# Kernel tuning notes

Measured on AMD Instinct MI355X. Metric: run time of the kernel, lower is better.

Reference implementation:

```python
import jax, jax.numpy as jnp
import numpy as np

B, CIN, CINT, H, W = 2, 2048, 512, 96, 96
CQK = CINT // 8  # 64, mmcv CrissCrossAttention query/key channels
NG = 32          # GroupNorm groups
EPS = 1e-5


def conv1x1(x, w, b):
    # x: [B,C,H,W], w: [O,C,1,1], b: [O]
    y = jnp.einsum('bchw,oc->bohw', x, w[:, :, 0, 0])
    return y + b[None, :, None, None]


def conv3x3(x, w):
    return jax.lax.conv_general_dilated(
        x, w, window_strides=(1, 1), padding=((1, 1), (1, 1)),
        dimension_numbers=('NCHW', 'OIHW', 'NCHW'))


def group_norm(x, gamma, beta):
    b, c, h, w = x.shape
    xg = x.reshape(b, NG, c // NG, h, w)
    mu = xg.mean(axis=(2, 3, 4), keepdims=True)
    var = xg.var(axis=(2, 3, 4), keepdims=True)
    xg = (xg - mu) * jax.lax.rsqrt(var + EPS)
    return xg.reshape(b, c, h, w) * gamma[None, :, None, None] + beta[None, :, None, None]


def criss_cross_attention(x, qw, qb, kw, kb, vw, vb, gamma):
    # mmcv CrissCrossAttention: attention restricted to each pixel's row + column.
    b, c, h, w = x.shape
    q = conv1x1(x, qw, qb)  # [B,Cqk,H,W]
    k = conv1x1(x, kw, kb)  # [B,Cqk,H,W]
    v = conv1x1(x, vw, vb)  # [B,C,H,W]
    # column (H-direction) energy: e_H[b,h,w,i] = sum_c q[b,c,h,w] k[b,c,i,w]
    e_h = jnp.einsum('bchw,bciw->bhwi', q, k)
    diag = jnp.eye(h, dtype=bool)[:, None, :]  # mask i==h (self counted once, in W branch)
    e_h = jnp.where(diag, -jnp.inf, e_h)
    # row (W-direction) energy: e_W[b,h,w,j] = sum_c q[b,c,h,w] k[b,c,h,j]
    e_w = jnp.einsum('bchw,bchj->bhwj', q, k)
    attn = jax.nn.softmax(jnp.concatenate([e_h, e_w], axis=-1), axis=-1)  # [B,H,W,H+W]
    a_h, a_w = attn[..., :h], attn[..., h:]
    out = jnp.einsum('bciw,bhwi->bchw', v, a_h) + jnp.einsum('bchj,bhwj->bchw', v, a_w)
    return gamma * out + x


def setup_inputs() -> dict:
    key = jax.random.key(0)
    ks = jax.random.split(key, 12)
    s = 0.02
    return {
        'x': jax.random.normal(ks[0], (B, CIN, H, W), jnp.float32),
        'conv1_w': jax.random.normal(ks[1], (CINT, CIN, 1, 1), jnp.float32) * s,
        'conv1_b': jnp.zeros((CINT,), jnp.float32),
        'q_w': jax.random.normal(ks[2], (CQK, CINT, 1, 1), jnp.float32) * s,
        'q_b': jnp.zeros((CQK,), jnp.float32),
        'k_w': jax.random.normal(ks[3], (CQK, CINT, 1, 1), jnp.float32) * s,
        'k_b': jnp.zeros((CQK,), jnp.float32),
        'v_w': jax.random.normal(ks[4], (CINT, CINT, 1, 1), jnp.float32) * s,
        'v_b': jnp.zeros((CINT,), jnp.float32),
        'gamma': jnp.asarray(0.5, jnp.float32),
        'convout_w': jax.random.normal(ks[5], (CINT, CINT, 3, 3), jnp.float32) * s,
        'gn_gamma': jnp.ones((CINT,), jnp.float32),
        'gn_beta': jnp.zeros((CINT,), jnp.float32),
    }


def reference(x, conv1_w, conv1_b, q_w, q_b, k_w, k_b, v_w, v_b, gamma,
              convout_w, gn_gamma, gn_beta):
    out = conv1x1(x, conv1_w, conv1_b)
    for _ in range(2):  # recurrence = 2
        out = criss_cross_attention(out, q_w, q_b, k_w, k_b, v_w, v_b, gamma)
    out = conv3x3(out, convout_w)  # ConvModule with GN => conv has no bias
    out = group_norm(out, gn_gamma, gn_beta)
    return out
```

## Files before the change

### kernel.cpp

```cpp
#include <hip/hip_runtime.h>
#include <hip/hip_bf16.h>


typedef __bf16 bf8_t __attribute__((ext_vector_type(8)));
typedef float f32x4 __attribute__((ext_vector_type(4)));

union I4B8 { int4 i; bf8_t b; };

typedef const __attribute__((address_space(1))) void as1_cvoid;
typedef __attribute__((address_space(3))) void as3_void;
__device__ __forceinline__ void gload16(const void* g, void* l) {
  __builtin_amdgcn_global_load_lds((as1_cvoid*)g, (as3_void*)l, 16, 0, 0);
}
__device__ __forceinline__ int rot8(int c, int key) { return (c + key) & 7; }

__global__ __launch_bounds__(256) void cast_rot_k(const float* s, __bf16* d, int K8, int total8) {
  int idx = blockIdx.x * 256 + threadIdx.x;
  if (idx >= total8) return;
  int c8 = idx % K8, n = idx / K8;
  int pos = rot8(c8 & 7, n & 7);
  const float* sp = s + ((long long)n * K8 + c8) * 8;
  float4 a = *(const float4*)sp, b = *(const float4*)(sp + 4);
  I4B8 u;
  u.b[0] = (__bf16)a.x; u.b[1] = (__bf16)a.y; u.b[2] = (__bf16)a.z; u.b[3] = (__bf16)a.w;
  u.b[4] = (__bf16)b.x; u.b[5] = (__bf16)b.y; u.b[6] = (__bf16)b.z; u.b[7] = (__bf16)b.w;
  *(int4*)(d + ((long long)n * K8 + (c8 & ~7) + pos) * 8) = u.i;
}

__global__ __launch_bounds__(256) void wqkv_rot_k(const float* qw, const float* kw, const float* vw, __bf16* d) {
  int idx = blockIdx.x * 256 + threadIdx.x;
  if (idx >= 640 * 64) return;
  int c8 = idx & 63, n = idx >> 6;
  const float* src = (n < 64) ? qw + (long long)n * 512
                   : (n < 128) ? kw + (long long)(n - 64) * 512
                               : vw + (long long)(n - 128) * 512;
  int pos = rot8(c8 & 7, n & 7);
  const float* sp = src + c8 * 8;
  float4 a = *(const float4*)sp, b = *(const float4*)(sp + 4);
  I4B8 u;
  u.b[0] = (__bf16)a.x; u.b[1] = (__bf16)a.y; u.b[2] = (__bf16)a.z; u.b[3] = (__bf16)a.w;
  u.b[4] = (__bf16)b.x; u.b[5] = (__bf16)b.y; u.b[6] = (__bf16)b.z; u.b[7] = (__bf16)b.w;
  *(int4*)(d + ((long long)n * 64 + (c8 & ~7) + pos) * 8) = u.i;
}

__global__ __launch_bounds__(256) void fuse_bias_k(const float* qb, const float* kb, const float* vb, float* d) {
  int i = blockIdx.x * 256 + threadIdx.x;
  if (i >= 640) return;
  d[i] = (i < 64) ? qb[i] : (i < 128) ? kb[i - 64] : vb[i - 128];
}

__global__ __launch_bounds__(256) void reorder_w_k(const float* w, __bf16* wr) {
  __shared__ float ls[4608];
  int o = blockIdx.x;
  int t = threadIdx.x;
  const float* base = w + (long long)o * 4608;
#pragma unroll
  for (int i = 0; i < 18; i++) ls[t + i * 256] = base[t + i * 256];
  __syncthreads();
#pragma unroll
  for (int i = 0; i < 3; i++) {
    int q = t + i * 256;
    if (q >= 576) break;
    int k0 = q * 8;
    int dydx = k0 / 512, c0 = k0 & 511;
    I4B8 u;
#pragma unroll
    for (int j = 0; j < 8; j++) u.b[j] = (__bf16)ls[(c0 + j) * 9 + dydx];
    int pos = rot8((k0 >> 3) & 7, o & 7);
    *(int4*)(wr + (long long)o * 4608 + (k0 & ~63) + pos * 8) = u.i;
  }
}

__global__ __launch_bounds__(256) void transpose_x_k(const float* x, __bf16* xt) {
  __shared__ __bf16 l[64 * 66];
  int c0 = blockIdx.x * 64, s0 = blockIdx.y * 64, b = blockIdx.z;
  int t = threadIdx.x;
#pragma unroll
  for (int i = 0; i < 2; i++) {
    int slot = t + i * 256;
    int cl = slot >> 3, sch = slot & 7;
    const float* src = x + ((long long)(b * 2048 + c0 + cl)) * 9216 + s0 + sch * 8;
    float4 a = *(const float4*)src, bb = *(const float4*)(src + 4);
    __bf16* dst = &l[cl * 66 + sch * 8];
    dst[0] = (__bf16)a.x; dst[1] = (__bf16)a.y; dst[2] = (__bf16)a.z; dst[3] = (__bf16)a.w;
    dst[4] = (__bf16)bb.x; dst[5] = (__bf16)bb.y; dst[6] = (__bf16)bb.z; dst[7] = (__bf16)bb.w;
  }
  __syncthreads();
#pragma unroll
  for (int i = 0; i < 2; i++) {
    int slot = t + i * 256;
    int sl = slot >> 3, cch = slot & 7;
    I4B8 u;
#pragma unroll
    for (int j = 0; j < 8; j++) u.b[j] = l[(cch * 8 + j) * 66 + sl];
    *(int4*)(xt + ((long long)(b * 9216 + s0 + sl)) * 2048 + c0 + rot8(cch, sl & 7) * 8) = u.i;
  }
}

__global__ __launch_bounds__(256) void border0_k(__bf16* padb) {
  int idx = blockIdx.x * 256 + threadIdx.x;
  if (idx >= 776 * 64) return;
  int ch = idx & 63, bi = idx >> 6;
  int b = bi / 388, r = bi % 388;
  int hh, ww;
  if (r < 98) { hh = 0; ww = r; }
  else if (r < 196) { hh = 97; ww = r - 98; }
  else if (r < 292) { hh = r - 196 + 1; ww = 0; }
  else { hh = r - 292 + 1; ww = 97; }
  *(int4*)(padb + ((long long)(b * 9604 + hh * 98 + ww)) * 512 + ch * 8) = make_int4(0, 0, 0, 0);
}

struct GemmAP {
  const __bf16 *A, *B;
  __bf16* C;
  const float* bias;
  long long sAr, sBr, sCr;
  int K, ntn;
};

template <int CROT>
__global__ __launch_bounds__(256) void gemm_async_k(GemmAP p) {
  __shared__ __attribute__((aligned(16))) __bf16 lA[128 * 64];
  __shared__ __attribute__((aligned(16))) __bf16 lB[128 * 64];
  const int t = threadIdx.x;
  const int id = blockIdx.x;
  const int per8 = gridDim.x >> 3;
  const int lin = (id & 7) * per8 + (id >> 3);
  const int m0 = (lin / p.ntn) * 128, n0 = (lin % p.ntn) * 128;
  const int lane = t & 63, wave = t >> 6;
  const int wm = (wave >> 1) * 64, wn = (wave & 1) * 64;
  const int l15 = lane & 15, l4 = lane >> 4;
  const int srow = (lane >> 3), schunk = (lane & 7) * 8;
  f32x4 acc[4][4];
#pragma unroll
  for (int i = 0; i < 4; i++)
#pragma unroll
    for (int j = 0; j < 4; j++) acc[i][j] = f32x4{0.f, 0.f, 0.f, 0.f};

  for (int kb = 0; kb < p.K; kb += 64) {
    const int rb = wave * 32;
#pragma unroll
    for (int i = 0; i < 4; i++) {
      int row = rb + i * 8;
      gload16(p.A + (long long)(m0 + row + srow) * p.sAr + kb + schunk, &lA[row * 64]);
      gload16(p.B + (long long)(n0 + row + srow) * p.sBr + kb + schunk, &lB[row * 64]);
    }
    __syncthreads();
#pragma unroll
    for (int kk = 0; kk < 2; kk++) {
      bf8_t af[4], bfr[4];
      int cch = kk * 4 + l4;
#pragma unroll
      for (int mt = 0; mt < 4; mt++) {
        int r = wm + mt * 16 + l15;
        af[mt] = *(bf8_t*)&lA[r * 64 + (rot8(cch, r & 7) << 3)];
      }
#pragma unroll
      for (int nt = 0; nt < 4; nt++) {
        int r = wn + nt * 16 + l15;
        bfr[nt] = *(bf8_t*)&lB[r * 64 + (rot8(cch, r & 7) << 3)];
      }
#pragma unroll
      for (int mt = 0; mt < 4; mt++)
#pragma unroll
        for (int nt = 0; nt < 4; nt++)
          acc[mt][nt] = __builtin_amdgcn_mfma_f32_16x16x32_bf16(af[mt], bfr[nt], acc[mt][nt], 0, 0, 0);
    }
    __syncthreads();
  }
#pragma unroll
  for (int nt = 0; nt < 4; nt++) {
    int col = n0 + wn + nt * 16 + l15;
    float bv = p.bias[col];
#pragma unroll
    for (int mt = 0; mt < 4; mt++) {
      int row0 = m0 + wm + mt * 16 + (l4 << 2);
#pragma unroll
      for (int r = 0; r < 4; r++) {
        int row = row0 + r;
        int pc = CROT ? (col & ~63) + (rot8((col >> 3) & 7, row & 7) << 3) + (col & 7) : col;
        p.C[(long long)row * p.sCr + pc] = (__bf16)(acc[mt][nt][r] + bv);
      }
    }
  }
}

struct AggP {
  const __bf16 *A, *B;
  __bf16* C;
  const __bf16 *tmp, *res;
  const float* gma;
  long long bB1, bB2, sBr;
  long long cB1, cB2, sCr;
};

template <int MODE>
__global__ __launch_bounds__(256) void agg_k(AggP p) {
  __shared__ __attribute__((aligned(16))) __bf16 lA[128 * 64];
  __shared__ __attribute__((aligned(16))) __bf16 lB[128 * 64];
  const int t = threadIdx.x;
  const int z = blockIdx.z;
  const int z1 = z / 96, z2 = z % 96;
  const __bf16* A = p.A + (long long)z * (96 * 128);
  const __bf16* B = p.B + (long long)z1 * p.bB1 + (long long)z2 * p.bB2;
  const int n0 = blockIdx.x * 128;
  const int lane = t & 63, wave = t >> 6;
  const int wm = (wave >> 1) * 64, wn = (wave & 1) * 64;
  const int l15 = lane & 15, l4 = lane >> 4;
  const int srow = lane >> 3, schunk = (lane & 7) * 8;
  f32x4 acc[4][4];
#pragma unroll
  for (int i = 0; i < 4; i++)
#pragma unroll
    for (int j = 0; j < 4; j++) acc[i][j] = f32x4{0.f, 0.f, 0.f, 0.f};

#pragma unroll
  for (int kb = 0; kb < 128; kb += 64) {
    const int rb = wave * 32;
#pragma unroll
    for (int i = 0; i < 4; i++) {
      int row = rb + i * 8;
      gload16(A + (long long)(row + srow) * 128 + kb + schunk, &lA[row * 64]);
    }
#pragma unroll
    for (int i = 0; i < 4; i++) {
      int slot = t + i * 256;
      int kl = slot & 63, cch = slot >> 6;
      int gk = kb + kl;
      I4B8 u;
      u.i = make_int4(0, 0, 0, 0);
      if (gk < 96) u.i = *(const int4*)(B + (long long)gk * p.sBr + n0 + cch * 8);
#pragma unroll
      for (int j = 0; j < 8; j++) {
        int n = cch * 8 + j;
        lB[n * 64 + (rot8(kl >> 3, n & 7) << 3) + (kl & 7)] = u.b[j];
      }
    }
    __syncthreads();
#pragma unroll
    for (int kk = 0; kk < 2; kk++) {
      bf8_t af[4], bfr[4];
      int cch = kk * 4 + l4;
#pragma unroll
      for (int mt = 0; mt < 4; mt++) {
        int r = wm + mt * 16 + l15;
        af[mt] = *(bf8_t*)&lA[r * 64 + (rot8(cch, r & 7) << 3)];
      }
#pragma unroll
      for (int nt = 0; nt < 4; nt++) {
        int r = wn + nt * 16 + l15;
        bfr[nt] = *(bf8_t*)&lB[r * 64 + (rot8(cch, r & 7) << 3)];
      }
#pragma unroll
      for (int mt = 0; mt < 4; mt++)
#pragma unroll
        for (int nt = 0; nt < 4; nt++)
          acc[mt][nt] = __builtin_amdgcn_mfma_f32_16x16x32_bf16(af[mt], bfr[nt], acc[mt][nt], 0, 0, 0);
    }
    __syncthreads();
  }
  long long cbase = (long long)z1 * p.cB1 + (long long)z2 * p.cB2;
  float g = MODE ? *p.gma : 0.f;
#pragma unroll
  for (int nt = 0; nt < 4; nt++) {
    int col = n0 + wn + nt * 16 + l15;
#pragma unroll
    for (int mt = 0; mt < 4; mt++) {
      int row0 = wm + mt * 16 + (l4 << 2);
#pragma unroll
      for (int r = 0; r < 4; r++) {
        int row = row0 + r;
        if (row >= 96) continue;
        long long offL = cbase + (long long)row * p.sCr + col;
        float v = acc[mt][nt][r];
        if (MODE == 0) {
          p.C[offL] = (__bf16)v;
        } else {
          int rc = (col & ~63) + (rot8((col >> 3) & 7, row & 7) << 3) + (col & 7);
          long long offP = cbase + (long long)row * p.sCr + rc;
          v = g * ((float)p.tmp[offL] + v) + (float)p.res[offP];
          if (MODE == 1) {
            p.C[offP] = (__bf16)v;
          } else {
            int pc = (col & ~63) + (rot8((col >> 3) & 7, (row + 1) & 7) << 3) + (col & 7);
            long long pidx = (long long)z1 * 9604 + (long long)(z2 + 1) * 98 + (row + 1);
            p.C[pidx * 512 + pc] = (__bf16)v;
          }
        }
      }
    }
  }
}

__global__ __launch_bounds__(384) void cc_scores_k(const __bf16* qkv, float* attnfH, float* attnfW) {
  __shared__ __attribute__((aligned(16))) __bf16 Qs[96 * 64];
  __shared__ __attribute__((aligned(16))) __bf16 Ks[96 * 64];
  int bfi = blockIdx.x;
  int b = bfi / 96, f = bfi % 96;
  int mode = blockIdx.y;
  long long base = (mode == 0) ? ((long long)(b * 9216 + f)) * 640 : ((long long)(b * 9216 + f * 96)) * 640;
  long long rstr = (mode == 0) ? 96 * 640 : 640;
  int t = threadIdx.x;
#pragma unroll
  for (int i = 0; i < 2; i++) {
    int slot = t + i * 384;
    int r = slot >> 3, c = slot & 7;
    int sw = rot8(c, r & 7) << 3;
    *(int4*)&Qs[r * 64 + sw] = *(const int4*)(qkv + base + (long long)r * rstr + c * 8);
    *(int4*)&Ks[r * 64 + sw] = *(const int4*)(qkv + base + (long long)r * rstr + 64 + c * 8);
  }
  __syncthreads();
  int lane = t & 63, wave = t >> 6;
  int l15 = lane & 15, l4 = lane >> 4;
  f32x4 acc[6];
#pragma unroll
  for (int i = 0; i < 6; i++) acc[i] = f32x4{0.f, 0.f, 0.f, 0.f};
#pragma unroll
  for (int kk = 0; kk < 2; kk++) {
    int ar = wave * 16 + l15;
    int cch = kk * 4 + l4;
    bf8_t af = *(bf8_t*)&Qs[ar * 64 + (rot8(cch, ar & 7) << 3)];
#pragma unroll
    for (int nt = 0; nt < 6; nt++) {
      int br = nt * 16 + l15;
      bf8_t bfr = *(bf8_t*)&Ks[br * 64 + (rot8(cch, br & 7) << 3)];
      acc[nt] = __builtin_amdgcn_mfma_f32_16x16x32_bf16(af, bfr, acc[nt], 0, 0, 0);
    }
  }
  float* dst = (mode == 0 ? attnfH : attnfW) + (long long)bfi * 9216;
#pragma unroll
  for (int nt = 0; nt < 6; nt++) {
#pragma unroll
    for (int r = 0; r < 4; r++) {
      int m = wave * 16 + (l4 << 2) + r;
      int n = nt * 16 + l15;
      float v = acc[nt][r];
      if (mode == 0 && n == m) v = -__builtin_inff();
      dst[m * 96 + n] = v;
    }
  }
}

__global__ __launch_bounds__(256) void cc_softmax_k(const float* attnfH, const float* attnfW,
                                                    __bf16* a_h, __bf16* a_w) {
  int wave = threadIdx.x >> 6, lane = threadIdx.x & 63;
  int pix = blockIdx.x * 4 + wave;
  int b = pix / 9216, hw = pix % 9216;
  int h = hw / 96, w2 = hw % 96;
  const float* ehb = attnfH + ((long long)(b * 96 + w2)) * 9216 + h * 96;
  const float* ewb = attnfW + ((long long)(b * 96 + h)) * 9216 + w2 * 96;
  float x0 = ehb[lane];
  float x1 = lane < 32 ? ehb[64 + lane] : -__builtin_inff();
  float x2 = ewb[lane];
  float x3 = lane < 32 ? ewb[64 + lane] : -__builtin_inff();
  float m = fmaxf(fmaxf(x0, x1), fmaxf(x2, x3));
#pragma unroll
  for (int o = 32; o; o >>= 1) m = fmaxf(m, __shfl_xor(m, o));
  float e0 = __expf(x0 - m), e1 = __expf(x1 - m), e2 = __expf(x2 - m), e3 = __expf(x3 - m);
  float s = e0 + e1 + e2 + e3;
#pragma unroll
  for (int o = 32; o; o >>= 1) s += __shfl_xor(s, o);
  float inv = 1.f / s;
  __bf16* dh = a_h + ((long long)((b * 96 + w2) * 96 + h)) * 128;
  __bf16* dw = a_w + ((long long)((b * 96 + h) * 96 + w2)) * 128;
  int kh = h & 7, kw2 = w2 & 7;
  int k1 = lane, k2 = 64 + lane;
  int p1h = (k1 & ~63) + (rot8((k1 >> 3) & 7, kh) << 3) + (k1 & 7);
  int p2h = (k2 & ~63) + (rot8((k2 >> 3) & 7, kh) << 3) + (k2 & 7);
  int p1w = (k1 & ~63) + (rot8((k1 >> 3) & 7, kw2) << 3) + (k1 & 7);
  int p2w = (k2 & ~63) + (rot8((k2 >> 3) & 7, kw2) << 3) + (k2 & 7);
  dh[p1h] = (__bf16)(e0 * inv);
  dh[p2h] = (__bf16)(lane < 32 ? e1 * inv : 0.f);
  dw[p1w] = (__bf16)(e2 * inv);
  dw[p2w] = (__bf16)(lane < 32 ? e3 * inv : 0.f);
}

__global__ __launch_bounds__(256) void conv3_gemm_k(const __bf16* pin, const __bf16* wr, __bf16* C) {
  __shared__ __attribute__((aligned(16))) __bf16 lA[128 * 64];
  __shared__ __attribute__((aligned(16))) __bf16 lB[128 * 64];
  const int t = threadIdx.x;
  const int id = blockIdx.x;
  const int per8 = gridDim.x >> 3;
  const int lin = (id & 7) * per8 + (id >> 3);
  const int m0 = (lin >> 2) * 128, n0 = (lin & 3) * 128;
  const int lane = t & 63, wave = t >> 6;
  const int wm = (wave >> 1) * 64, wn = (wave & 1) * 64;
  const int l15 = lane & 15, l4 = lane >> 4;
  const int srow = lane >> 3, schunk = (lane & 7) * 8;
  const int rb = wave * 32;
  f32x4 acc[4][4];
#pragma unroll
  for (int i = 0; i < 4; i++)
#pragma unroll
    for (int j = 0; j < 4; j++) acc[i][j] = f32x4{0.f, 0.f, 0.f, 0.f};
  long long sbase[4], bbase[4];
#pragma unroll
  for (int i = 0; i < 4; i++) {
    int r = rb + i * 8 + srow;
    int m = m0 + r;
    int b = m / 9216, hw = m % 9216;
    int h = hw / 96, w2 = hw % 96;
    sbase[i] = ((long long)b * 9604 + h * 98 + w2) * 512 + schunk;
    bbase[i] = (long long)(n0 + r) * 4608 + schunk;
  }
  int w2f[4];
#pragma unroll
  for (int mt = 0; mt < 4; mt++) w2f[mt] = (m0 + wm + mt * 16 + l15) % 96;

  int kt = 0;
  for (int tap = 0; tap < 9; tap++) {
    const int dy = tap / 3, dx = tap - dy * 3;
    const long long aoff = (long long)(dy * 98 + dx) * 512;
    int keyA[4];
#pragma unroll
    for (int mt = 0; mt < 4; mt++) keyA[mt] = (w2f[mt] + dx) & 7;
    for (int sl = 0; sl < 8; sl++, kt++) {
      const int c0k = sl * 64;
#pragma unroll
      for (int i = 0; i < 4; i++) {
        gload16(pin + sbase[i] + aoff + c0k, &lA[(rb + i * 8) * 64]);
        gload16(wr + bbase[i] + kt * 64, &lB[(rb + i * 8) * 64]);
      }
      __syncthreads();
#pragma unroll
      for (int kk = 0; kk < 2; kk++) {
        bf8_t af[4], bfr[4];
        int cch = kk * 4 + l4;
#pragma unroll
        for (int mt = 0; mt < 4; mt++) {
          int r = wm + mt * 16 + l15;
          af[mt] = *(bf8_t*)&lA[r * 64 + (rot8(cch, keyA[mt]) << 3)];
        }
#pragma unroll
        for (int nt = 0; nt < 4; nt++) {
          int r = wn + nt * 16 + l15;
          bfr[nt] = *(bf8_t*)&lB[r * 64 + (rot8(cch, r & 7) << 3)];
        }
#pragma unroll
        for (int mt = 0; mt < 4; mt++)
#pragma unroll
          for (int nt = 0; nt < 4; nt++)
            acc[mt][nt] = __builtin_amdgcn_mfma_f32_16x16x32_bf16(af[mt], bfr[nt], acc[mt][nt], 0, 0, 0);
      }
      __syncthreads();
    }
  }
#pragma unroll
  for (int nt = 0; nt < 4; nt++) {
    int col = n0 + wn + nt * 16 + l15;
#pragma unroll
    for (int mt = 0; mt < 4; mt++) {
      int row0 = m0 + wm + mt * 16 + (l4 << 2);
#pragma unroll
      for (int r = 0; r < 4; r++) {
        int row = row0 + r;
        C[(long long)row * 512 + col] = (__bf16)acc[mt][nt][r];
      }
    }
  }
}

__global__ __launch_bounds__(256) void gn_stats_k(const __bf16* z, float* stats) {
  int bg = blockIdx.x;
  int b = bg >> 5, g = bg & 31;
  int t = threadIdx.x;
  int cch = t & 1, sp0 = t >> 1;
  const __bf16* base = z + (long long)b * 9216 * 512 + g * 16 + cch * 8;
  float s = 0.f, ss = 0.f;
  for (int sp = sp0; sp < 9216; sp += 128) {
    I4B8 u;
    u.i = *(const int4*)(base + (long long)sp * 512);
#pragma unroll
    for (int j = 0; j < 8; j++) {
      float f = (float)u.b[j];
      s += f;
      ss += f * f;
    }
  }
#pragma unroll
  for (int o = 32; o; o >>= 1) {
    s += __shfl_xor(s, o);
    ss += __shfl_xor(ss, o);
  }
  __shared__ float red[8];
  int wave = t >> 6, lane = t & 63;
  if (lane == 0) {
    red[wave] = s;
    red[4 + wave] = ss;
  }
  __syncthreads();
  if (t == 0) {
    float S = red[0] + red[1] + red[2] + red[3];
    float SS = red[4] + red[5] + red[6] + red[7];
    const float inv = 1.f / 147456.f;
    float mean = S * inv;
    float var = SS * inv - mean * mean;
    stats[2 * bg] = mean;
    stats[2 * bg + 1] = rsqrtf(var + 1e-5f);
  }
}

__global__ __launch_bounds__(256) void gn_write_k(const __bf16* z, const float* stats,
                                                 const float* gng, const float* gnb, float* out) {
  __shared__ __bf16 l[64 * 98];
  int c0 = blockIdx.x * 64, h = blockIdx.y, b = blockIdx.z;
  int t = threadIdx.x;
#pragma unroll
  for (int i = 0; i < 3; i++) {
    int slot = t + i * 256;
    int wl = slot >> 3, cch = slot & 7;
    I4B8 u;
    u.i = *(const int4*)(z + ((long long)(b * 9216 + h * 96 + wl)) * 512 + c0 + cch * 8);
#pragma unroll
    for (int j = 0; j < 8; j++) l[(cch * 8 + j) * 98 + wl] = u.b[j];
  }
  __syncthreads();
#pragma unroll
  for (int i = 0; i < 3; i++) {
    int slot = t + i * 256;
    int wch = slot % 12, cl = slot / 12;
    int c = c0 + cl;
    int g = c >> 4;
    float mean = stats[2 * (b * 32 + g)], rstd = stats[2 * (b * 32 + g) + 1];
    float sc = rstd * gng[c];
    float sh = gnb[c] - mean * sc;
    float4 o0, o1;
    const __bf16* src = &l[cl * 98 + wch * 8];
    o0.x = (float)src[0] * sc + sh; o0.y = (float)src[1] * sc + sh;
    o0.z = (float)src[2] * sc + sh; o0.w = (float)src[3] * sc + sh;
    o1.x = (float)src[4] * sc + sh; o1.y = (float)src[5] * sc + sh;
    o1.z = (float)src[6] * sc + sh; o1.w = (float)src[7] * sc + sh;
    float* dst = out + ((long long)((b * 512 + c) * 96 + h)) * 96 + wch * 8;
    *(float4*)dst = o0;
    *(float4*)(dst + 4) = o1;
  }
}

extern "C" void kernel_launch(void* const* d_in, const int* in_sizes, int n_in,
                              void* d_out, int out_size, void* d_ws, size_t ws_size,
                              hipStream_t stream) {
  (void)in_sizes; (void)n_in; (void)out_size;
  const float* x = (const float*)d_in[0];
  const float* conv1w = (const float*)d_in[1];
  const float* conv1b = (const float*)d_in[2];
  const float* qw = (const float*)d_in[3];
  const float* qbias = (const float*)d_in[4];
  const float* kw = (const float*)d_in[5];
  const float* kbias = (const float*)d_in[6];
  const float* vw = (const float*)d_in[7];
  const float* vbias = (const float*)d_in[8];
  const float* gma = (const float*)d_in[9];
  const float* cow = (const float*)d_in[10];
  const float* gng = (const float*)d_in[11];
  const float* gnb = (const float*)d_in[12];
  float* out = (float*)d_out;

  if (ws_size < 134876160ULL) return;

  char* w = (char*)d_ws;
  __bf16* xt     = (__bf16*)(w);
  __bf16* qkv    = (__bf16*)(w);
  float* attnfH  = (float*)(w + 23592960);
  float* attnfW  = (float*)(w + 30670848);
  __bf16* a_h    = (__bf16*)(w + 37748736);
  __bf16* a_w    = (__bf16*)(w + 42467328);
  __bf16* padb   = (__bf16*)(w + 47185920);
  __bf16* wrot   = (__bf16*)(w + 66854912);
  __bf16* ya     = (__bf16*)(w + 75497472);
  __bf16* yb     = (__bf16*)(w + 94371840);
  __bf16* tmp1   = (__bf16*)(w + 113246208);
  __bf16* zb     = (__bf16*)(w);
  __bf16* c1wb   = (__bf16*)(w + 132120576);
  __bf16* wqkvb  = (__bf16*)(w + 134217728);
  float* qkvbias = (float*)(w + 134873088);
  float* stats   = (float*)(w + 134875648);

  cast_rot_k<<<512, 256, 0, stream>>>(conv1w, c1wb, 256, 131072);
  wqkv_rot_k<<<160, 256, 0, stream>>>(qw, kw, vw, wqkvb);
  fuse_bias_k<<<3, 256, 0, stream>>>(qbias, kbias, vbias, qkvbias);
  transpose_x_k<<<dim3(32, 144, 2), 256, 0, stream>>>(x, xt);

  {
    GemmAP p{};
    p.A = xt; p.B = c1wb; p.C = ya; p.bias = conv1b;
    p.sAr = 2048; p.sBr = 2048; p.sCr = 512;
    p.K = 2048; p.ntn = 4;
    gemm_async_k<1><<<576, 256, 0, stream>>>(p);
  }

  for (int it = 0; it < 2; it++) {
    __bf16* tin = it ? yb : ya;
    {
      GemmAP p{};
      p.A = tin; p.B = wqkvb; p.C = qkv; p.bias = qkvbias;
      p.sAr = 512; p.sBr = 512; p.sCr = 640;
      p.K = 512; p.ntn = 5;
      gemm_async_k<0><<<720, 256, 0, stream>>>(p);
    }
    cc_scores_k<<<dim3(192, 2), 384, 0, stream>>>(qkv, attnfH, attnfW);
    cc_softmax_k<<<4608, 256, 0, stream>>>(attnfH, attnfW, a_h, a_w);
    {
      AggP p{};
      p.A = a_h; p.B = qkv + 128; p.C = tmp1;
      p.bB1 = (long long)9216 * 640; p.bB2 = 640; p.sBr = (long long)96 * 640;
      p.cB1 = (long long)9216 * 512; p.cB2 = 512; p.sCr = (long long)96 * 512;
      agg_k<0><<<dim3(4, 1, 192), 256, 0, stream>>>(p);
    }
    {
      AggP p{};
      p.A = a_w; p.B = qkv + 128;
      p.bB1 = (long long)9216 * 640; p.bB2 = (long long)96 * 640; p.sBr = 640;
      p.cB1 = (long long)9216 * 512; p.cB2 = (long long)96 * 512; p.sCr = 512;
      p.tmp = tmp1; p.res = tin; p.gma = gma;
      if (it == 0) {
        p.C = yb;
        agg_k<1><<<dim3(4, 1, 192), 256, 0, stream>>>(p);
      } else {
        p.C = padb;
        agg_k<2><<<dim3(4, 1, 192), 256, 0, stream>>>(p);
      }
    }
  }

  reorder_w_k<<<512, 256, 0, stream>>>(cow, wrot);
  border0_k<<<194, 256, 0, stream>>>(padb);
  conv3_gemm_k<<<576, 256, 0, stream>>>(padb, wrot, zb);
  gn_stats_k<<<64, 256, 0, stream>>>(zb, stats);
  gn_write_k<<<dim3(8, 96, 2), 256, 0, stream>>>(zb, stats, gng, gnb, out);
}
```

Measured before the change: 662.6 us.

## Halve GEMM N-tile and parallelize GroupNorm stats with atomics

The 1x1-conv GEMM tile shrinks from 128x128 to 128x64, doubling the grid for the conv1 and qkv projections so more blocks fill the CUs. GroupNorm statistics move from 64 blocks, each striding over a whole group, to 256 blocks over contiguous spatial chunks. These blocks accumulate per-group sums and sums of squares with atomicAdd into a buffer zeroed in the bias kernel, and mean and rstd are now computed in the write kernel. Smaller tiles cost more operand reloads, and the atomic float sums make the statistics order-dependent.

```diff
diff --git a/kernel.cpp b/kernel.cpp
--- a/kernel.cpp
+++ b/kernel.cpp
@@ -43,8 +43,10 @@
   *(int4*)(d + ((long long)n * 64 + (c8 & ~7) + pos) * 8) = u.i;
 }
 
-__global__ __launch_bounds__(256) void fuse_bias_k(const float* qb, const float* kb, const float* vb, float* d) {
+__global__ __launch_bounds__(256) void fuse_bias_k(const float* qb, const float* kb, const float* vb,
+                                                   float* d, float* stats) {
   int i = blockIdx.x * 256 + threadIdx.x;
+  if (i < 128) stats[i] = 0.f;
   if (i >= 640) return;
   d[i] = (i < 64) ? qb[i] : (i < 128) ? kb[i - 64] : vb[i - 128];
 }
@@ -121,34 +123,38 @@
 template <int CROT>
 __global__ __launch_bounds__(256) void gemm_async_k(GemmAP p) {
   __shared__ __attribute__((aligned(16))) __bf16 lA[128 * 64];
-  __shared__ __attribute__((aligned(16))) __bf16 lB[128 * 64];
+  __shared__ __attribute__((aligned(16))) __bf16 lB[64 * 64];
   const int t = threadIdx.x;
   const int id = blockIdx.x;
   const int per8 = gridDim.x >> 3;
   const int lin = (id & 7) * per8 + (id >> 3);
-  const int m0 = (lin / p.ntn) * 128, n0 = (lin % p.ntn) * 128;
+  const int m0 = (lin / p.ntn) * 128, n0 = (lin % p.ntn) * 64;
   const int lane = t & 63, wave = t >> 6;
-  const int wm = (wave >> 1) * 64, wn = (wave & 1) * 64;
+  const int wm = (wave >> 1) * 64, wn = (wave & 1) * 32;
   const int l15 = lane & 15, l4 = lane >> 4;
   const int srow = (lane >> 3), schunk = (lane & 7) * 8;
-  f32x4 acc[4][4];
+  f32x4 acc[4][2];
 #pragma unroll
   for (int i = 0; i < 4; i++)
 #pragma unroll
-    for (int j = 0; j < 4; j++) acc[i][j] = f32x4{0.f, 0.f, 0.f, 0.f};
+    for (int j = 0; j < 2; j++) acc[i][j] = f32x4{0.f, 0.f, 0.f, 0.f};
 
   for (int kb = 0; kb < p.K; kb += 64) {
-    const int rb = wave * 32;
+    const int rbA = wave * 32, rbB = wave * 16;
 #pragma unroll
     for (int i = 0; i < 4; i++) {
-      int row = rb + i * 8;
+      int row = rbA + i * 8;
       gload16(p.A + (long long)(m0 + row + srow) * p.sAr + kb + schunk, &lA[row * 64]);
+    }
+#pragma unroll
+    for (int i = 0; i < 2; i++) {
+      int row = rbB + i * 8;
       gload16(p.B + (long long)(n0 + row + srow) * p.sBr + kb + schunk, &lB[row * 64]);
     }
     __syncthreads();
 #pragma unroll
     for (int kk = 0; kk < 2; kk++) {
-      bf8_t af[4], bfr[4];
+      bf8_t af[4], bfr[2];
       int cch = kk * 4 + l4;
 #pragma unroll
       for (int mt = 0; mt < 4; mt++) {
@@ -156,20 +162,20 @@
         af[mt] = *(bf8_t*)&lA[r * 64 + (rot8(cch, r & 7) << 3)];
       }
 #pragma unroll
-      for (int nt = 0; nt < 4; nt++) {
+      for (int nt = 0; nt < 2; nt++) {
         int r = wn + nt * 16 + l15;
         bfr[nt] = *(bf8_t*)&lB[r * 64 + (rot8(cch, r & 7) << 3)];
       }
 #pragma unroll
       for (int mt = 0; mt < 4; mt++)
 #pragma unroll
-        for (int nt = 0; nt < 4; nt++)
+        for (int nt = 0; nt < 2; nt++)
           acc[mt][nt] = __builtin_amdgcn_mfma_f32_16x16x32_bf16(af[mt], bfr[nt], acc[mt][nt], 0, 0, 0);
     }
     __syncthreads();
   }
 #pragma unroll
-  for (int nt = 0; nt < 4; nt++) {
+  for (int nt = 0; nt < 2; nt++) {
     int col = n0 + wn + nt * 16 + l15;
     float bv = p.bias[col];
 #pragma unroll
@@ -461,15 +467,14 @@
 }
 
 __global__ __launch_bounds__(256) void gn_stats_k(const __bf16* z, float* stats) {
-  int bg = blockIdx.x;
-  int b = bg >> 5, g = bg & 31;
-  int t = threadIdx.x;
-  int cch = t & 1, sp0 = t >> 1;
-  const __bf16* base = z + (long long)b * 9216 * 512 + g * 16 + cch * 8;
+  int bi = blockIdx.x, t = threadIdx.x;
+  const __bf16* base = z + (long long)bi * (72 * 512);
+  int g = (t & 63) >> 1;
   float s = 0.f, ss = 0.f;
-  for (int sp = sp0; sp < 9216; sp += 128) {
+#pragma unroll
+  for (int i = 0; i < 18; i++) {
     I4B8 u;
-    u.i = *(const int4*)(base + (long long)sp * 512);
+    u.i = *(const int4*)(base + ((long long)(t + i * 256)) * 8);
 #pragma unroll
     for (int j = 0; j < 8; j++) {
       float f = (float)u.b[j];
@@ -477,26 +482,21 @@
       ss += f * f;
     }
   }
-#pragma unroll
-  for (int o = 32; o; o >>= 1) {
-    s += __shfl_xor(s, o);
-    ss += __shfl_xor(ss, o);
-  }
-  __shared__ float red[8];
+  s += __shfl_xor(s, 1);
+  ss += __shfl_xor(ss, 1);
+  __shared__ float red[2][4][32];
   int wave = t >> 6, lane = t & 63;
-  if (lane == 0) {
-    red[wave] = s;
-    red[4 + wave] = ss;
+  if (!(lane & 1)) {
+    red[0][wave][g] = s;
+    red[1][wave][g] = ss;
   }
   __syncthreads();
-  if (t == 0) {
-    float S = red[0] + red[1] + red[2] + red[3];
-    float SS = red[4] + red[5] + red[6] + red[7];
-    const float inv = 1.f / 147456.f;
-    float mean = S * inv;
-    float var = SS * inv - mean * mean;
-    stats[2 * bg] = mean;
-    stats[2 * bg + 1] = rsqrtf(var + 1e-5f);
+  if (t < 32) {
+    float S = red[0][0][t] + red[0][1][t] + red[0][2][t] + red[0][3][t];
+    float SS = red[1][0][t] + red[1][1][t] + red[1][2][t] + red[1][3][t];
+    int b = bi >> 7;
+    atomicAdd(&stats[2 * (b * 32 + t)], S);
+    atomicAdd(&stats[2 * (b * 32 + t) + 1], SS);
   }
 }
 
@@ -515,13 +515,16 @@
     for (int j = 0; j < 8; j++) l[(cch * 8 + j) * 98 + wl] = u.b[j];
   }
   __syncthreads();
+  const float inv = 1.f / 147456.f;
 #pragma unroll
   for (int i = 0; i < 3; i++) {
     int slot = t + i * 256;
     int wch = slot % 12, cl = slot / 12;
     int c = c0 + cl;
     int g = c >> 4;
-    float mean = stats[2 * (b * 32 + g)], rstd = stats[2 * (b * 32 + g) + 1];
+    float S = stats[2 * (b * 32 + g)], SS = stats[2 * (b * 32 + g) + 1];
+    float mean = S * inv;
+    float rstd = rsqrtf(SS * inv - mean * mean + 1e-5f);
     float sc = rstd * gng[c];
     float sh = gnb[c] - mean * sc;
     float4 o0, o1;
@@ -577,15 +580,15 @@
 
   cast_rot_k<<<512, 256, 0, stream>>>(conv1w, c1wb, 256, 131072);
   wqkv_rot_k<<<160, 256, 0, stream>>>(qw, kw, vw, wqkvb);
-  fuse_bias_k<<<3, 256, 0, stream>>>(qbias, kbias, vbias, qkvbias);
+  fuse_bias_k<<<3, 256, 0, stream>>>(qbias, kbias, vbias, qkvbias, stats);
   transpose_x_k<<<dim3(32, 144, 2), 256, 0, stream>>>(x, xt);
 
   {
     GemmAP p{};
     p.A = xt; p.B = c1wb; p.C = ya; p.bias = conv1b;
     p.sAr = 2048; p.sBr = 2048; p.sCr = 512;
-    p.K = 2048; p.ntn = 4;
-    gemm_async_k<1><<<576, 256, 0, stream>>>(p);
+    p.K = 2048; p.ntn = 8;
+    gemm_async_k<1><<<1152, 256, 0, stream>>>(p);
   }
 
   for (int it = 0; it < 2; it++) {
@@ -594,8 +597,8 @@
       GemmAP p{};
       p.A = tin; p.B = wqkvb; p.C = qkv; p.bias = qkvbias;
       p.sAr = 512; p.sBr = 512; p.sCr = 640;
-      p.K = 512; p.ntn = 5;
-      gemm_async_k<0><<<720, 256, 0, stream>>>(p);
+      p.K = 512; p.ntn = 10;
+      gemm_async_k<0><<<1440, 256, 0, stream>>>(p);
     }
     cc_scores_k<<<dim3(192, 2), 384, 0, stream>>>(qkv, attnfH, attnfW);
     cc_softmax_k<<<4608, 256, 0, stream>>>(attnfH, attnfW, a_h, a_w);
@@ -625,6 +628,6 @@
   reorder_w_k<<<512, 256, 0, stream>>>(cow, wrot);
   border0_k<<<194, 256, 0, stream>>>(padb);
   conv3_gemm_k<<<576, 256, 0, stream>>>(padb, wrot, zb);
-  gn_stats_k<<<64, 256, 0, stream>>>(zb, stats);
+  gn_stats_k<<<256, 256, 0, stream>>>(zb, stats);
   gn_write_k<<<dim3(8, 96, 2), 256, 0, stream>>>(zb, stats, gng, gnb, out);
 }
```

Measured after the change: 619.1 us. 6.6% less time.
